# Optimization experiments

Measured on AMD Instinct MI355X. Metric: run time of the kernel, lower is better.

## Reference

```python
import jax, jax.numpy as jnp
import numpy as np

B, S, D = 2, 2048, 1024
H = 16
DH = D // H  # 64


def setup_inputs() -> dict:
    key = jax.random.key(0)
    ks = jax.random.split(key, 6)
    sc = 0.02
    return {
        "x": jax.random.normal(ks[0], (B, S, D), dtype=jnp.float32),
        "Wq": jax.random.normal(ks[1], (D, D), dtype=jnp.float32) * sc,
        "Wk": jax.random.normal(ks[2], (D, D), dtype=jnp.float32) * sc,
        "Wv": jax.random.normal(ks[3], (D, D), dtype=jnp.float32) * sc,
        "Wo": jax.random.normal(ks[4], (D, D), dtype=jnp.float32) * sc,
        "bo": jnp.zeros((D,), dtype=jnp.float32),
    }


def reference(x, Wq, Wk, Wv, Wo, bo):
    b, s, _ = x.shape
    # project_qkv: Linear (x @ W.T), view to heads, transpose -> [b, H, s, DH]
    def split_heads(t):
        return t.reshape(b, s, H, DH).transpose(0, 2, 1, 3)

    q = split_heads(x @ Wq.T)
    k = split_heads(x @ Wk.T)
    v = split_heads(x @ Wv.T)

    # attn_scores = q @ k^T  [b, H, s, s]
    scores = jnp.einsum("bhqd,bhkd->bhqk", q, k)
    # causal mask: triu(ones, diagonal=1) -> mask out strictly-future positions
    causal = jnp.triu(jnp.ones((s, s), dtype=bool), k=1)
    scores = jnp.where(causal[None, None], -jnp.inf, scores)
    scale = 1.0 / jnp.sqrt(jnp.float32(DH))
    attn = jax.nn.softmax(scores * scale, axis=-1)
    # dropout p=0.0 -> identity
    ctx = jnp.einsum("bhqk,bhkd->bhqd", attn, v)
    # transpose back and flatten heads -> [b, s, D]
    ctx = ctx.transpose(0, 2, 1, 3).reshape(b, s, H * DH)
    return ctx @ Wo.T + bo
```

## Files before the change

### kernel.cpp

```cpp
#include <hip/hip_runtime.h>
#include <stdint.h>

typedef unsigned short u16;
typedef __attribute__((ext_vector_type(8))) short bf16x8;
typedef __attribute__((ext_vector_type(4))) float f32x4;
typedef __attribute__((ext_vector_type(4))) unsigned short u16x4;

__device__ __forceinline__ u16 f2bf(float f) {
  union { float f; uint32_t u; } c; c.f = f;
  uint32_t u = c.u;
  return (u16)((u + 0x7fffu + ((u >> 16) & 1u)) >> 16);
}

__device__ __forceinline__ uint32_t pk_bf16(float lo, float hi) {
  uint32_t d;
  asm("v_cvt_pk_bf16_f32 %0, %1, %2" : "=v"(d) : "v"(lo), "v"(hi));
  return d;
}

__device__ __forceinline__ void gload_lds16(const u16* g, u16* l) {
  __builtin_amdgcn_global_load_lds(
      (const __attribute__((address_space(1))) void*)g,
      (__attribute__((address_space(3))) void*)l, 16, 0, 0);
}

__global__ void cast_f32_bf16(const float* __restrict__ src, u16* __restrict__ dst, int n) {
  int i = (blockIdx.x * blockDim.x + threadIdx.x) * 4;
  int stride = gridDim.x * blockDim.x * 4;
  for (; i < n; i += stride) {
    float4 v = *reinterpret_cast<const float4*>(src + i);
    u16x4 o = { f2bf(v.x), f2bf(v.y), f2bf(v.z), f2bf(v.w) };
    *reinterpret_cast<u16x4*>(dst + i) = o;
  }
}

__global__ void cast_weights(const float* __restrict__ Wq, const float* __restrict__ Wk,
                             const float* __restrict__ Wv, const float* __restrict__ Wo,
                             u16* __restrict__ Wcat, u16* __restrict__ Wob) {
  int i = (blockIdx.x * blockDim.x + threadIdx.x) * 4;
  int stride = gridDim.x * blockDim.x * 4;
  for (; i < 4194304; i += stride) {
    const int sel = i >> 20;
    const int off = i & 1048575;
    const float* src = (sel == 0) ? Wq : (sel == 1) ? Wk : (sel == 2) ? Wv : Wo;
    float4 v = *reinterpret_cast<const float4*>(src + off);
    u16x4 o = { f2bf(v.x), f2bf(v.y), f2bf(v.z), f2bf(v.w) };
    u16* dst = (sel < 3) ? (Wcat + i) : (Wob + off);
    *reinterpret_cast<u16x4*>(dst) = o;
  }
}

#define QSCALE 0.18033688011112042f

template<int EPI>
__global__ __launch_bounds__(256) void gemm_bt(
    const u16* __restrict__ A, const u16* __restrict__ B,
    int M, int N, int K,
    u16* __restrict__ o0, u16* __restrict__ o1, u16* __restrict__ o2,
    float* __restrict__ fo, const float* __restrict__ bias)
{
  __shared__ __align__(16) u16 As[2][128 * 32];
  __shared__ __align__(16) u16 Bs[2][128 * 32];
  const int tid = threadIdx.x;
  const int w = tid >> 6, l = tid & 63;
  const int m0 = blockIdx.y * 128, n0 = blockIdx.x * 128;
  const int arow = (w << 4) + (l >> 2);
  const int acol = (l & 3) << 3;
  const int wr = (w >> 1) << 6, wc = (w & 1) << 6;
  const int lr = l & 15, hi = l >> 4;
  const int lk = hi << 3;
  f32x4 acc[4][4] = {};

  const u16* Ap = A + (size_t)(m0 + arow) * K + acol;
  const u16* Bp = B + (size_t)(n0 + arow) * K + acol;
  const int so = (w << 9);

  gload_lds16(Ap, &As[0][so]);
  gload_lds16(Ap + (size_t)64 * K, &As[0][so + 2048]);
  gload_lds16(Bp, &Bs[0][so]);
  gload_lds16(Bp + (size_t)64 * K, &Bs[0][so + 2048]);

  int buf = 0;
  for (int k0 = 0; k0 < K; k0 += 32) {
    if (k0 + 32 < K) {
      const int nb = buf ^ 1;
      gload_lds16(Ap + k0 + 32, &As[nb][so]);
      gload_lds16(Ap + (size_t)64 * K + k0 + 32, &As[nb][so + 2048]);
      gload_lds16(Bp + k0 + 32, &Bs[nb][so]);
      gload_lds16(Bp + (size_t)64 * K + k0 + 32, &Bs[nb][so + 2048]);
      asm volatile("s_waitcnt vmcnt(4)" ::: "memory");
    } else {
      asm volatile("s_waitcnt vmcnt(0)" ::: "memory");
    }
    __builtin_amdgcn_sched_barrier(0);
    __builtin_amdgcn_s_barrier();
    bf16x8 af[4], bfr[4];
#pragma unroll
    for (int m = 0; m < 4; ++m)
      af[m] = *(const bf16x8*)(&As[buf][0] + (wr + m * 16 + lr) * 32 + lk);
#pragma unroll
    for (int n = 0; n < 4; ++n)
      bfr[n] = *(const bf16x8*)(&Bs[buf][0] + (wc + n * 16 + lr) * 32 + lk);
    __builtin_amdgcn_s_setprio(1);
#pragma unroll
    for (int m = 0; m < 4; ++m)
#pragma unroll
      for (int n = 0; n < 4; ++n)
        acc[m][n] = __builtin_amdgcn_mfma_f32_16x16x32_bf16(af[m], bfr[n], acc[m][n], 0, 0, 0);
    __builtin_amdgcn_s_setprio(0);
    __builtin_amdgcn_s_barrier();
    buf ^= 1;
  }

#pragma unroll
  for (int mm = 0; mm < 4; ++mm) {
#pragma unroll
    for (int nn = 0; nn < 4; ++nn) {
      const int ng = n0 + wc + nn * 16 + lr;
      if (EPI == 0) {
        const int mat = ng >> 10;
        const int col = ng & 1023;
        const int h = col >> 6, dh = col & 63;
#pragma unroll
        for (int r = 0; r < 4; ++r) {
          const int mg = m0 + wr + mm * 16 + (hi << 2) + r;
          const int b = mg >> 11, s = mg & 2047;
          if (mat == 0)
            o0[(((size_t)(b * 16 + h)) * 2048 + s) * 64 + dh] = f2bf(acc[mm][nn][r] * QSCALE);
          else if (mat == 1)
            o1[(((size_t)(b * 16 + h)) * 2048 + s) * 64 + dh] = f2bf(acc[mm][nn][r]);
          else
            o2[(((size_t)(b * 16 + h)) * 64 + dh) * 2048 + s] = f2bf(acc[mm][nn][r]);
        }
      } else {
        const float bv = bias[ng];
#pragma unroll
        for (int r = 0; r < 4; ++r) {
          const int mg = m0 + wr + mm * 16 + (hi << 2) + r;
          fo[(size_t)mg * N + ng] = acc[mm][nn][r] + bv;
        }
      }
    }
  }
}

__global__ __launch_bounds__(256) void flash_attn(
    const u16* __restrict__ Qg, const u16* __restrict__ Kg,
    const u16* __restrict__ Vtg, u16* __restrict__ ctx)
{
  __shared__ __align__(16) u16 Ks[2][4096];
  __shared__ __align__(16) u16 Vts[2][4096];
  __shared__ __align__(16) u16 PT[4][1024];
  const int tid = threadIdx.x, w = tid >> 6, l = tid & 63;
  const int lr = l & 15, hi = l >> 4;
  const int x = blockIdx.x, y = blockIdx.y;
  const int xi = (x + y) & 31;
  const int qt = (xi & 1) ? (31 - (xi >> 1)) : (xi >> 1);
  const int bh = y;
  const size_t kqbase = (size_t)bh * (2048 * 64);
  const int q0 = qt * 64;
  const int nkt = qt + 1;

  bf16x8 qf[2];
  {
    const u16* qp = Qg + kqbase + (size_t)(q0 + w * 16 + lr) * 64 + hi * 8;
    qf[0] = *(const bf16x8*)(qp);
    qf[1] = *(const bf16x8*)(qp + 32);
  }

  const int c0 = (w * 2 + 0) * 64 + l;
  const int c1 = (w * 2 + 1) * 64 + l;
  const int r0 = c0 >> 3, p0 = c0 & 7;
  const int r1 = c1 >> 3, p1 = c1 & 7;
  const u16* kg0 = Kg + kqbase + r0 * 64 + ((p0 ^ (r0 & 7)) << 3);
  const u16* kg1 = Kg + kqbase + r1 * 64 + ((p1 ^ (r1 & 7)) << 3);
  const u16* vg0 = Vtg + kqbase + r0 * 2048 + ((p0 ^ (r0 & 7)) << 3);
  const u16* vg1 = Vtg + kqbase + r1 * 2048 + ((p1 ^ (r1 & 7)) << 3);
  u16* kd0 = (u16*)&Ks[0][(w * 2 + 0) * 512];
  u16* kd1 = (u16*)&Ks[0][(w * 2 + 1) * 512];
  u16* vd0 = (u16*)&Vts[0][(w * 2 + 0) * 512];
  u16* vd1 = (u16*)&Vts[0][(w * 2 + 1) * 512];

  f32x4 acc[4] = {};
  float lsum = 0.0f;
  const int qg = q0 + w * 16 + lr;

  gload_lds16(kg0, kd0);
  gload_lds16(kg1, kd1);
  gload_lds16(vg0, vd0);
  gload_lds16(vg1, vd1);

  int buf = 0;
  for (int kt = 0; kt < nkt; ++kt) {
    if (kt + 1 < nkt) {
      const int nb = (buf ^ 1) * 4096;
      gload_lds16(kg0 + (size_t)(kt + 1) * 4096, kd0 + nb);
      gload_lds16(kg1 + (size_t)(kt + 1) * 4096, kd1 + nb);
      gload_lds16(vg0 + (kt + 1) * 64, vd0 + nb);
      gload_lds16(vg1 + (kt + 1) * 64, vd1 + nb);
      asm volatile("s_waitcnt vmcnt(8)" ::: "memory");
    } else {
      asm volatile("s_waitcnt vmcnt(0)" ::: "memory");
    }
    __builtin_amdgcn_sched_barrier(0);
    __builtin_amdgcn_s_barrier();
    {
      const u16* ksb = &Ks[buf][0];
      const u16* vsb = &Vts[buf][0];
      f32x4 sv[4];
      __builtin_amdgcn_s_setprio(1);
#pragma unroll
      for (int cf = 0; cf < 4; ++cf) {
        f32x4 z = {};
#pragma unroll
        for (int ch = 0; ch < 2; ++ch) {
          const int krow = cf * 16 + lr;
          const int boff = ((krow << 7) + ((ch * 32 + hi * 8) << 1)) ^ ((krow & 7) << 4);
          bf16x8 kf = *(const bf16x8*)((const char*)ksb + boff);
          z = __builtin_amdgcn_mfma_f32_16x16x32_bf16(kf, qf[ch], z, 0, 0, 0);
        }
        sv[cf] = z;
      }
      __builtin_amdgcn_s_setprio(0);

      const bool diag = (kt == nkt - 1);
      const int kb = kt * 64 + hi * 4;
      float ts = 0.0f;
#pragma unroll
      for (int cf = 0; cf < 4; ++cf) {
        f32x4 pv;
#pragma unroll
        for (int r = 0; r < 4; ++r) {
          float s = sv[cf][r];
          if (diag && (kb + cf * 16 + r) > qg) s = -1e30f;
          pv[r] = exp2f(s);
        }
        sv[cf] = pv;
        ts += (pv[0] + pv[1]) + (pv[2] + pv[3]);
      }
      lsum += ts;

      {
        const int rowb = lr << 7;
        const int swz = (lr & 7) << 4;
#pragma unroll
        for (int cf = 0; cf < 4; ++cf) {
          uint32_t d0 = pk_bf16(sv[cf][0], sv[cf][1]);
          uint32_t d1 = pk_bf16(sv[cf][2], sv[cf][3]);
          uint2 val = { d0, d1 };
          const int boff = (rowb + ((cf * 16 + hi * 4) << 1)) ^ swz;
          *(uint2*)((char*)&PT[w][0] + boff) = val;
        }
      }

#pragma unroll
      for (int ch = 0; ch < 2; ++ch) {
        const int boffp = ((lr << 7) + (ch * 64 + hi * 16)) ^ ((lr & 7) << 4);
        bf16x8 pa = *(const bf16x8*)((const char*)&PT[w][0] + boffp);
        __builtin_amdgcn_s_setprio(1);
#pragma unroll
        for (int df = 0; df < 4; ++df) {
          const int vrow = df * 16 + lr;
          const int boffv = ((vrow << 7) + ((ch * 32 + hi * 8) << 1)) ^ ((vrow & 7) << 4);
          bf16x8 vf = *(const bf16x8*)((const char*)vsb + boffv);
          acc[df] = __builtin_amdgcn_mfma_f32_16x16x32_bf16(pa, vf, acc[df], 0, 0, 0);
        }
        __builtin_amdgcn_s_setprio(0);
      }
    }
    __builtin_amdgcn_s_barrier();
    buf ^= 1;
  }

  float lf = lsum;
  lf += __shfl_xor(lf, 16);
  lf += __shfl_xor(lf, 32);
  const int h = bh & 15, b = bh >> 4;
#pragma unroll
  for (int r = 0; r < 4; ++r) {
    const float inv = 1.0f / __shfl(lf, hi * 4 + r);
    const int s = q0 + w * 16 + hi * 4 + r;
    const size_t rowbase = ((size_t)(b * 2048 + s)) * 1024 + h * 64;
#pragma unroll
    for (int df = 0; df < 4; ++df)
      ctx[rowbase + df * 16 + lr] = f2bf(acc[df][r] * inv);
  }
}

extern "C" void kernel_launch(void* const* d_in, const int* in_sizes, int n_in,
                              void* d_out, int out_size, void* d_ws, size_t ws_size,
                              hipStream_t stream) {
  const float* x  = (const float*)d_in[0];
  const float* Wq = (const float*)d_in[1];
  const float* Wk = (const float*)d_in[2];
  const float* Wv = (const float*)d_in[3];
  const float* Wo = (const float*)d_in[4];
  const float* bo = (const float*)d_in[5];
  float* out = (float*)d_out;

  const size_t MB = 1ull << 20;
  if (ws_size < 48 * MB) return;
  char* ws = (char*)d_ws;
  u16* xb   = (u16*)(ws);
  u16* Wcat = (u16*)(ws + 8 * MB);
  u16* Wob  = (u16*)(ws + 14 * MB);
  u16* Qb   = (u16*)(ws + 16 * MB);
  u16* Kb   = (u16*)(ws + 24 * MB);
  u16* Vtb  = (u16*)(ws + 32 * MB);
  u16* ctxb = (u16*)(ws + 40 * MB);

  hipLaunchKernelGGL(cast_f32_bf16, dim3(2048), dim3(256), 0, stream, x, xb, 4194304);
  hipLaunchKernelGGL(cast_weights, dim3(2048), dim3(256), 0, stream,
                     Wq, Wk, Wv, Wo, Wcat, Wob);

  hipLaunchKernelGGL((gemm_bt<0>), dim3(24, 32), dim3(256), 0, stream,
                     xb, Wcat, 4096, 3072, 1024, Qb, Kb, Vtb, (float*)nullptr, (const float*)nullptr);
  hipLaunchKernelGGL(flash_attn, dim3(32, 32), dim3(256), 0, stream, Qb, Kb, Vtb, ctxb);
  hipLaunchKernelGGL((gemm_bt<1>), dim3(8, 32), dim3(256), 0, stream,
                     ctxb, Wob, 4096, 1024, 1024,
                     (u16*)nullptr, (u16*)nullptr, (u16*)nullptr, out, bo);
}
```

Measured before the change: 142.0 us.

## Fuse cast kernels, remap attention blocks per XCD, tighten prefetch wait

Merges the separate input and weight cast kernels into one launch, saving a kernel launch and its tail. Flattens the flash-attention grid and remaps block IDs so that all q-tiles of a given batch-head land on the same XCD, aiming for better L2 reuse of K/V. It also changes the prefetch waitcnt from vmcnt(8) to vmcnt(4), which waits more conservatively for loads already issued. That may add stall time but fixes a possible ordering issue.

```diff
diff --git a/kernel.cpp b/kernel.cpp
--- a/kernel.cpp
+++ b/kernel.cpp
@@ -24,28 +24,25 @@
       (__attribute__((address_space(3))) void*)l, 16, 0, 0);
 }
 
-__global__ void cast_f32_bf16(const float* __restrict__ src, u16* __restrict__ dst, int n) {
+__global__ void cast_all(const float* __restrict__ x,
+                         const float* __restrict__ Wq, const float* __restrict__ Wk,
+                         const float* __restrict__ Wv, const float* __restrict__ Wo,
+                         u16* __restrict__ xb, u16* __restrict__ Wcat, u16* __restrict__ Wob) {
   int i = (blockIdx.x * blockDim.x + threadIdx.x) * 4;
-  int stride = gridDim.x * blockDim.x * 4;
-  for (; i < n; i += stride) {
-    float4 v = *reinterpret_cast<const float4*>(src + i);
+  const int stride = gridDim.x * blockDim.x * 4;
+  for (; i < 8388608; i += stride) {
+    const float* src;
+    u16* dst;
+    if (i < 4194304) {
+      src = x + i; dst = xb + i;
+    } else {
+      const int j = i - 4194304;
+      const int sel = j >> 20, off = j & 1048575;
+      src = ((sel == 0) ? Wq : (sel == 1) ? Wk : (sel == 2) ? Wv : Wo) + off;
+      dst = (sel < 3) ? (Wcat + j) : (Wob + off);
+    }
+    float4 v = *reinterpret_cast<const float4*>(src);
     u16x4 o = { f2bf(v.x), f2bf(v.y), f2bf(v.z), f2bf(v.w) };
-    *reinterpret_cast<u16x4*>(dst + i) = o;
-  }
-}
-
-__global__ void cast_weights(const float* __restrict__ Wq, const float* __restrict__ Wk,
-                             const float* __restrict__ Wv, const float* __restrict__ Wo,
-                             u16* __restrict__ Wcat, u16* __restrict__ Wob) {
-  int i = (blockIdx.x * blockDim.x + threadIdx.x) * 4;
-  int stride = gridDim.x * blockDim.x * 4;
-  for (; i < 4194304; i += stride) {
-    const int sel = i >> 20;
-    const int off = i & 1048575;
-    const float* src = (sel == 0) ? Wq : (sel == 1) ? Wk : (sel == 2) ? Wv : Wo;
-    float4 v = *reinterpret_cast<const float4*>(src + off);
-    u16x4 o = { f2bf(v.x), f2bf(v.y), f2bf(v.z), f2bf(v.w) };
-    u16* dst = (sel < 3) ? (Wcat + i) : (Wob + off);
     *reinterpret_cast<u16x4*>(dst) = o;
   }
 }
@@ -153,10 +150,11 @@
   __shared__ __align__(16) u16 PT[4][1024];
   const int tid = threadIdx.x, w = tid >> 6, l = tid & 63;
   const int lr = l & 15, hi = l >> 4;
-  const int x = blockIdx.x, y = blockIdx.y;
-  const int xi = (x + y) & 31;
-  const int qt = (xi & 1) ? (31 - (xi >> 1)) : (xi >> 1);
-  const int bh = y;
+  const int bid = blockIdx.x;
+  const int xcd = bid & 7, j = bid >> 3;
+  const int bh = xcd + ((j >> 5) << 3);
+  const int qts = j & 31;
+  const int qt = (qts & 1) ? (31 - (qts >> 1)) : (qts >> 1);
   const size_t kqbase = (size_t)bh * (2048 * 64);
   const int q0 = qt * 64;
   const int nkt = qt + 1;
@@ -174,8 +172,8 @@
   const int r1 = c1 >> 3, p1 = c1 & 7;
   const u16* kg0 = Kg + kqbase + r0 * 64 + ((p0 ^ (r0 & 7)) << 3);
   const u16* kg1 = Kg + kqbase + r1 * 64 + ((p1 ^ (r1 & 7)) << 3);
-  const u16* vg0 = Vtg + kqbase + r0 * 2048 + ((p0 ^ (r0 & 7)) << 3);
-  const u16* vg1 = Vtg + kqbase + r1 * 2048 + ((p1 ^ (r1 & 7)) << 3);
+  const u16* vg0 = Vtg + kqbase + (size_t)r0 * 2048 + ((p0 ^ (r0 & 7)) << 3);
+  const u16* vg1 = Vtg + kqbase + (size_t)r1 * 2048 + ((p1 ^ (r1 & 7)) << 3);
   u16* kd0 = (u16*)&Ks[0][(w * 2 + 0) * 512];
   u16* kd1 = (u16*)&Ks[0][(w * 2 + 1) * 512];
   u16* vd0 = (u16*)&Vts[0][(w * 2 + 0) * 512];
@@ -198,7 +196,7 @@
       gload_lds16(kg1 + (size_t)(kt + 1) * 4096, kd1 + nb);
       gload_lds16(vg0 + (kt + 1) * 64, vd0 + nb);
       gload_lds16(vg1 + (kt + 1) * 64, vd1 + nb);
-      asm volatile("s_waitcnt vmcnt(8)" ::: "memory");
+      asm volatile("s_waitcnt vmcnt(4)" ::: "memory");
     } else {
       asm volatile("s_waitcnt vmcnt(0)" ::: "memory");
     }
@@ -309,13 +307,11 @@
   u16* Vtb  = (u16*)(ws + 32 * MB);
   u16* ctxb = (u16*)(ws + 40 * MB);
 
-  hipLaunchKernelGGL(cast_f32_bf16, dim3(2048), dim3(256), 0, stream, x, xb, 4194304);
-  hipLaunchKernelGGL(cast_weights, dim3(2048), dim3(256), 0, stream,
-                     Wq, Wk, Wv, Wo, Wcat, Wob);
-
+  hipLaunchKernelGGL(cast_all, dim3(4096), dim3(256), 0, stream,
+                     x, Wq, Wk, Wv, Wo, xb, Wcat, Wob);
   hipLaunchKernelGGL((gemm_bt<0>), dim3(24, 32), dim3(256), 0, stream,
                      xb, Wcat, 4096, 3072, 1024, Qb, Kb, Vtb, (float*)nullptr, (const float*)nullptr);
-  hipLaunchKernelGGL(flash_attn, dim3(32, 32), dim3(256), 0, stream, Qb, Kb, Vtb, ctxb);
+  hipLaunchKernelGGL(flash_attn, dim3(1024), dim3(256), 0, stream, Qb, Kb, Vtb, ctxb);
   hipLaunchKernelGGL((gemm_bt<1>), dim3(8, 32), dim3(256), 0, stream,
                      ctxb, Wob, 4096, 1024, 1024,
                      (u16*)nullptr, (u16*)nullptr, (u16*)nullptr, out, bo);
```

Result: slower. 146.6 us (+3.2%).
